# Kernel optimization log

Measured on AMD Instinct MI355X. Metric: run time of the kernel, lower is better.

## Reference

```python
import jax, jax.numpy as jnp
import numpy as np
from jax import lax

MAX_NUM_LEVELS = 3.5
MIN_LEVEL = 0.0
# torch computes num_levels = ceil(levels.max())+1 (data-dependent); since levels are
# clamped to max_num_levels-1 = 2.5, the static upper bound is ceil(2.5)+1 = 4.
# Building the full stack is mathematically identical (gather selects the same levels).
NUM_LEVELS = int(np.ceil(MAX_NUM_LEVELS - 1.0)) + 1  # = 4


def _blur_filter():
    f = np.array([1.0, 3.0, 3.0, 1.0])
    k = f[:, None] * f[None, :]
    k = k / k.sum()
    return jnp.asarray(k, jnp.float32)  # [4,4]


def _downsample_2x(x):
    # reflect-pad 1, depthwise 4x4 Gaussian conv, stride 2  -> [N,C,H/2,W/2]
    N, C, H, W = x.shape
    k = jnp.tile(_blur_filter()[None, None], (C, 1, 1, 1))  # [C,1,4,4]
    xp = jnp.pad(x, ((0, 0), (0, 0), (1, 1), (1, 1)), mode='reflect')
    return lax.conv_general_dilated(xp, k.astype(x.dtype), (2, 2), 'VALID',
                                    feature_group_count=C)


def _upsample(x, scale):
    # bilinear, align_corners=False (half-pixel centers) == jax.image.resize 'bilinear'
    N, C, H, W = x.shape
    return jax.image.resize(x, (N, C, int(H * scale), int(W * scale)), method='bilinear')


def _max_coord_distance(coords):
    # coords [N,H,W,2] -> max neighbor distance [N,H,W] (replication-padded neighbors)
    cp = jnp.pad(coords, ((0, 0), (1, 1), (1, 1), (0, 0)), mode='edge')
    cl = cp[:, 1:-1, :-2]
    cr = cp[:, 1:-1, 2:]
    cu = cp[:, :-2, 1:-1]
    cd = cp[:, 2:, 1:-1]

    def _dist(o):
        sq = jnp.sum((o - coords) ** 2, axis=-1)
        return jnp.sqrt(jnp.clip(sq, 1.0, None))

    return jnp.maximum(jnp.maximum(_dist(cl), _dist(cr)),
                       jnp.maximum(_dist(cu), _dist(cd)))


def _grid_sample_border(img, grid):
    # img [N,K,H,W], grid [N,Ho,Wo,2] in [-1,1]; bilinear, align_corners=False,
    # padding_mode='border' (coords clamped to valid range before interpolation)
    N, K, H, W = img.shape
    ix = jnp.clip(((grid[..., 0] + 1.0) * W - 1.0) / 2.0, 0.0, W - 1.0)
    iy = jnp.clip(((grid[..., 1] + 1.0) * H - 1.0) / 2.0, 0.0, H - 1.0)
    x0f, y0f = jnp.floor(ix), jnp.floor(iy)
    wx = (ix - x0f)[:, None]  # [N,1,Ho,Wo]
    wy = (iy - y0f)[:, None]
    x0 = x0f.astype(jnp.int32)
    y0 = y0f.astype(jnp.int32)
    x1 = jnp.clip(x0 + 1, 0, W - 1)
    y1 = jnp.clip(y0 + 1, 0, H - 1)

    def _gather(im, yi, xi):  # im [K,H,W] -> [K,Ho,Wo]
        return im[:, yi, xi]

    g = jax.vmap(_gather)
    v00 = g(img, y0, x0)
    v01 = g(img, y0, x1)
    v10 = g(img, y1, x0)
    v11 = g(img, y1, x1)
    return (v00 * (1 - wx) + v01 * wx) * (1 - wy) + (v10 * (1 - wx) + v11 * wx) * wy


def setup_inputs() -> dict:
    key = jax.random.key(0)
    k1, k2 = jax.random.split(key)
    N, C, H, W = 4, 96, 256, 256
    inputs = jax.random.normal(k1, (N, C, H, W), dtype=jnp.float32)
    # identity grid + mild random warp -> realistic spread of LOD levels
    ys = (jnp.arange(H, dtype=jnp.float32) + 0.5) / H * 2.0 - 1.0
    xs = (jnp.arange(W, dtype=jnp.float32) + 0.5) / W * 2.0 - 1.0
    gy, gx = jnp.meshgrid(ys, xs, indexing='ij')
    ident = jnp.stack([gx, gy], axis=-1)[None]  # [1,H,W,2]
    noise = (jax.random.uniform(k2, (N, H, W, 2), dtype=jnp.float32) * 2.0 - 1.0) * 0.05
    grid = jnp.clip(ident + noise, -1.0, 1.0)
    return {"inputs": inputs, "grid": grid}


def reference(inputs, grid):
    N, C, H, W = inputs.shape
    Ho, Wo = grid.shape[1], grid.shape[2]
    # absolute-pixel coords of the sampling grid
    xc = (W - 1.0) * (grid[..., 0] + 1.0) / 2.0
    yc = (H - 1.0) * (grid[..., 1] + 1.0) / 2.0
    coords = jnp.stack([xc, yc], axis=-1)  # [N,Ho,Wo,2]
    levels = jnp.clip(jnp.log2(_max_coord_distance(coords)), 0.0, MAX_NUM_LEVELS - 1.0)
    levels = jnp.clip(levels, MIN_LEVEL, None)  # [N,Ho,Wo]

    # Gaussian stack: blur+downsample, then bilinear-upsample back to full res
    lvl_imgs = [inputs]
    cur = inputs
    for i in range(1, NUM_LEVELS):
        cur = _downsample_2x(cur)
        lvl_imgs.append(_upsample(cur, 2.0 ** i))
    stack = jnp.stack(lvl_imgs, axis=2)  # [N,C,D,H,W]
    D = stack.shape[2]

    # warp all levels at once
    warped = _grid_sample_border(stack.reshape(N, C * D, H, W), grid)
    warped = warped.reshape(N, C, D, Ho, Wo)

    # per-pixel trilinear LOD blend
    l0 = jnp.floor(levels).astype(jnp.int32)
    l1 = jnp.ceil(levels).astype(jnp.int32)
    idx0 = jnp.broadcast_to(l0[:, None, None], (N, C, 1, Ho, Wo))
    idx1 = jnp.broadcast_to(l1[:, None, None], (N, C, 1, Ho, Wo))
    o0 = jnp.take_along_axis(warped, idx0, axis=2)[:, :, 0]
    o1 = jnp.take_along_axis(warped, idx1, axis=2)[:, :, 0]
    w = (levels - jnp.floor(levels))[:, None]  # [N,1,Ho,Wo], == levels % 1.0
    return o0 + w * (o1 - o0)
```

## Files before the change

kernel.cpp:

```cpp
#include <hip/hip_runtime.h>
#include <math.h>

namespace {

constexpr int N = 4, C = 96, H = 256, W = 256;
constexpr int HW = H * W;
constexpr float LMAX = 2.5f;

typedef float v4 __attribute__((ext_vector_type(4)));
struct __attribute__((packed, aligned(4))) V4U { v4 v; };
__device__ inline v4 load4u(const float* p) {
  return reinterpret_cast<const V4U*>(p)->v;
}

__global__ __launch_bounds__(256) void levels_kernel(
    const float* __restrict__ grid, float* __restrict__ levels) {
  int idx = blockIdx.x * 256 + threadIdx.x;
  int x = idx & (W - 1);
  int y = (idx >> 8) & (H - 1);
  int n = idx >> 16;
  const float2* gb = reinterpret_cast<const float2*>(grid) + (size_t)n * HW;

  auto cget = [&](int yy, int xx, float& cx, float& cy) {
    yy = min(max(yy, 0), H - 1);
    xx = min(max(xx, 0), W - 1);
    float2 g = gb[yy * W + xx];
    cx = (float)(W - 1) * (g.x + 1.0f) * 0.5f;
    cy = (float)(H - 1) * (g.y + 1.0f) * 0.5f;
  };

  float cx, cy;
  cget(y, x, cx, cy);
  float m = 1.0f;
  const int dxs[4] = {-1, 1, 0, 0};
  const int dys[4] = {0, 0, -1, 1};
#pragma unroll
  for (int i = 0; i < 4; i++) {
    float ox, oy;
    cget(y + dys[i], x + dxs[i], ox, oy);
    float dx = ox - cx, dy = oy - cy;
    m = fmaxf(m, dx * dx + dy * dy);
  }
  float lv = 0.5f * __log2f(m);
  lv = fminf(fmaxf(lv, 0.0f), LMAX);
  levels[idx] = lv;
}

__global__ __launch_bounds__(256) void downsample_tiled(
    const float* __restrict__ in, float* __restrict__ out, int Wi, int T) {
  __shared__ float s[68 * 68];
  int Wo = Wi >> 1;
  int tile = blockIdx.x;
  int nc = blockIdx.y;
  int tx0 = (tile % T) * 32, ty0 = (tile / T) * 32;
  int ix0 = 2 * tx0 - 2, iy0 = 2 * ty0 - 2;
  const float* p = in + (size_t)nc * Wi * Wi;
  int tid = threadIdx.x;

  for (int k = 0; k < 19; k++) {
    int e = tid + 256 * k;
    if (e < 68 * 68) {
      int yy = e / 68, xx = e - 68 * yy;
      int gy = iy0 + yy; gy = gy < 0 ? -gy : (gy >= Wi ? 2 * Wi - 2 - gy : gy);
      int gx = ix0 + xx; gx = gx < 0 ? -gx : (gx >= Wi ? 2 * Wi - 2 - gx : gx);
      s[e] = p[(size_t)gy * Wi + gx];
    }
  }
  __syncthreads();

  const float fw[4] = {0.125f, 0.375f, 0.375f, 0.125f};
  int dx = tid & 31, dy0 = tid >> 5;
  float* po = out + (size_t)nc * Wo * Wo;
#pragma unroll
  for (int r = 0; r < 4; r++) {
    int dy = dy0 + 8 * r;
    float acc = 0.0f;
#pragma unroll
    for (int a = 0; a < 4; a++) {
      const float* row = s + (2 * dy + 1 + a) * 68 + 2 * dx + 1;
      float rsum = fmaf(fw[0], row[0],
                   fmaf(fw[1], row[1],
                   fmaf(fw[2], row[2], fw[3] * row[3])));
      acc = fmaf(fw[a], rsum, acc);
    }
    po[(size_t)(ty0 + dy) * Wo + tx0 + dx] = acc;
  }
}

__device__ inline void axis3(int q0, int q1, float wq, int l, int S,
                             int* ii, float* ww) {
  float inv = 1.0f / (float)(1 << l);
  float pos0 = ((float)q0 + 0.5f) * inv - 0.5f;
  float pos1 = ((float)q1 + 0.5f) * inv - 0.5f;
  int p0 = (int)floorf(pos0), p1 = (int)floorf(pos1);
  float f0 = pos0 - (float)p0, f1 = pos1 - (float)p1;
  int a0 = min(max(p0, 0), S - 1), a1 = min(max(p0 + 1, 0), S - 1);
  int b0 = min(max(p1, 0), S - 1), b1 = min(max(p1 + 1, 0), S - 1);
  int base = min(a0, b0);
  float w0 = 0.f, w1 = 0.f, w2 = 0.f;
  float v; int s;
  v = (1.0f - wq) * (1.0f - f0); s = a0 - base;
  w0 += (s == 0) ? v : 0.f; w1 += (s == 1) ? v : 0.f; w2 += (s == 2) ? v : 0.f;
  v = (1.0f - wq) * f0;          s = a1 - base;
  w0 += (s == 0) ? v : 0.f; w1 += (s == 1) ? v : 0.f; w2 += (s == 2) ? v : 0.f;
  v = wq * (1.0f - f1);          s = b0 - base;
  w0 += (s == 0) ? v : 0.f; w1 += (s == 1) ? v : 0.f; w2 += (s == 2) ? v : 0.f;
  v = wq * f1;                   s = b1 - base;
  w0 += (s == 0) ? v : 0.f; w1 += (s == 1) ? v : 0.f; w2 += (s == 2) ? v : 0.f;
  ii[0] = base;
  ii[1] = min(base + 1, S - 1);
  ii[2] = min(base + 2, S - 1);
  ww[0] = w0; ww[1] = w1; ww[2] = w2;
}

constexpr int L2OFF = 8192, L3OFF = 11392, LDSTOT = 12544;

__global__ __launch_bounds__(256, 3) void gather_tiled(
    const float* __restrict__ inputs, const float* __restrict__ grid,
    const float* __restrict__ levels, const float* __restrict__ pyr1,
    const float* __restrict__ pyr2, const float* __restrict__ pyr3,
    float* __restrict__ out) {
  __shared__ __align__(16) float lds[LDSTOT];
  int tile = blockIdx.x, g = blockIdx.y, n = blockIdx.z;
  int tx0 = (tile & 15) << 4, ty0 = (tile >> 4) << 4;
  int gb = g * 32;
  int tid = threadIdx.x;

  int px = tid & 15, py = tid >> 4;
  int x = tx0 + px, y = ty0 + py;
  int pidx = n * HW + y * W + x;
  float2 gxy = reinterpret_cast<const float2*>(grid)[pidx];
  float lv = levels[pidx];

  int rsx1 = min(max((tx0 >> 1) - 4, 0), 128 - 16);
  int rsy1 = min(max((ty0 >> 1) - 4, 0), 128 - 16);
  int rsx2 = min(max((tx0 >> 2) - 3, 0), 64 - 10);
  int rsy2 = min(max((ty0 >> 2) - 3, 0), 64 - 10);
  int rsx3 = min(max((tx0 >> 3) - 2, 0), 32 - 6);
  int rsy3 = min(max((ty0 >> 3) - 2, 0), 32 - 6);

  {
    const float* base = pyr1 + ((size_t)(n * C + gb)) * (128 * 128);
#pragma unroll
    for (int k = 0; k < 32; k++) {
      int e = tid + 256 * k;
      int c = e >> 8, tf = e & 255;
      int yy = tf >> 4, xx = tf & 15;
      float t = base[(size_t)c * (128 * 128) + (rsy1 + yy) * 128 + rsx1 + xx];
      lds[(c >> 2) * 1024 + tf * 4 + (c & 3)] = t;
    }
  }
  {
    const float* base = pyr2 + ((size_t)(n * C + gb)) * (64 * 64);
    for (int k = 0; k < 13; k++) {
      int e = tid + 256 * k;
      if (e < 3200) {
        int c = e / 100, tf = e - 100 * c;
        int yy = tf / 10, xx = tf - 10 * yy;
        float t = base[(size_t)c * (64 * 64) + (rsy2 + yy) * 64 + rsx2 + xx];
        lds[L2OFF + (c >> 2) * 400 + tf * 4 + (c & 3)] = t;
      }
    }
  }
  {
    const float* base = pyr3 + ((size_t)(n * C + gb)) * (32 * 32);
    for (int k = 0; k < 5; k++) {
      int e = tid + 256 * k;
      if (e < 1152) {
        int c = e / 36, tf = e - 36 * c;
        int yy = tf / 6, xx = tf - 6 * yy;
        float t = base[(size_t)c * (32 * 32) + (rsy3 + yy) * 32 + rsx3 + xx];
        lds[L3OFF + (c >> 2) * 144 + tf * 4 + (c & 3)] = t;
      }
    }
  }
  __syncthreads();

  float ix = fminf(fmaxf(fmaf(gxy.x + 1.0f, 128.0f, -0.5f), 0.0f), 255.0f);
  float iy = fminf(fmaxf(fmaf(gxy.y + 1.0f, 128.0f, -0.5f), 0.0f), 255.0f);
  int x0 = (int)floorf(ix); float wx = ix - (float)x0; int x1 = min(x0 + 1, 255);
  int y0 = (int)floorf(iy); float wy = iy - (float)y0; int y1 = min(y0 + 1, 255);

  float lf = floorf(lv);
  int l0 = (int)lf;
  float wl = lv - lf;
  int lB = l0 + 1;

  auto meta = [&](int l, int& off, int& sz, int& rw, int& rx, int& ry, int& S) {
    if (l == 1)      { off = 0;     sz = 256; rw = 16; rx = rsx1; ry = rsy1; S = 128; }
    else if (l == 2) { off = L2OFF; sz = 100; rw = 10; rx = rsx2; ry = rsy2; S = 64; }
    else             { off = L3OFF; sz = 36;  rw = 6;  rx = rsx3; ry = rsy3; S = 32; }
  };

  int offB, szB, rwB, rxB, ryB, SB;
  meta(lB, offB, szB, rwB, rxB, ryB, SB);
  int tfB[9]; float wB[9];
  {
    int xi[3]; float xw[3]; axis3(x0, x1, wx, lB, SB, xi, xw);
    int yi[3]; float yw[3]; axis3(y0, y1, wy, lB, SB, yi, yw);
#pragma unroll
    for (int r = 0; r < 3; r++)
#pragma unroll
      for (int cc = 0; cc < 3; cc++) {
        int ry_ = min(max(yi[r] - ryB, 0), rwB - 1);
        int rx_ = min(max(xi[cc] - rxB, 0), rwB - 1);
        tfB[r * 3 + cc] = ry_ * rwB + rx_;
        wB[r * 3 + cc] = yw[r] * xw[cc];
      }
  }

  float* po = out + ((size_t)(n * C + gb)) * HW + (size_t)y * W + x;

  if (l0 >= 1) {
    int offA, szA, rwA, rxA, ryA, SA;
    meta(l0, offA, szA, rwA, rxA, ryA, SA);
    int tfA[9]; float wA[9];
    {
      int xi[3]; float xw[3]; axis3(x0, x1, wx, l0, SA, xi, xw);
      int yi[3]; float yw[3]; axis3(y0, y1, wy, l0, SA, yi, yw);
#pragma unroll
      for (int r = 0; r < 3; r++)
#pragma unroll
        for (int cc = 0; cc < 3; cc++) {
          int ry_ = min(max(yi[r] - ryA, 0), rwA - 1);
          int rx_ = min(max(xi[cc] - rxA, 0), rwA - 1);
          tfA[r * 3 + cc] = ry_ * rwA + rx_;
          wA[r * 3 + cc] = yw[r] * xw[cc];
        }
    }
#pragma unroll
    for (int q = 0; q < 8; q++) {
      const float* pA = lds + offA + q * szA * 4;
      const float* pB = lds + offB + q * szB * 4;
      v4 accA = {0.f, 0.f, 0.f, 0.f};
      v4 accB = {0.f, 0.f, 0.f, 0.f};
#pragma unroll
      for (int t = 0; t < 9; t++)
        accA += *reinterpret_cast<const v4*>(pA + tfA[t] * 4) * wA[t];
#pragma unroll
      for (int t = 0; t < 9; t++)
        accB += *reinterpret_cast<const v4*>(pB + tfB[t] * 4) * wB[t];
      v4 o = accA + (accB - accA) * wl;
      float* pq = po + (size_t)(4 * q) * HW;
      pq[0] = o.x; pq[HW] = o.y; pq[2 * (size_t)HW] = o.z; pq[3 * (size_t)HW] = o.w;
    }
  } else {
    const float* inA = inputs + ((size_t)(n * C + gb)) * HW;
#pragma unroll 1
    for (int q = 0; q < 8; q++) {
      const float* pB = lds + offB + q * szB * 4;
      v4 accB = {0.f, 0.f, 0.f, 0.f};
#pragma unroll
      for (int t = 0; t < 9; t++)
        accB += *reinterpret_cast<const v4*>(pB + tfB[t] * 4) * wB[t];
      float av[4];
#pragma unroll
      for (int j = 0; j < 4; j++) {
        const float* ip = inA + (size_t)(4 * q + j) * HW;
        float v00 = ip[y0 * W + x0], v01 = ip[y0 * W + x1];
        float v10 = ip[y1 * W + x0], v11 = ip[y1 * W + x1];
        av[j] = (v00 * (1.f - wx) + v01 * wx) * (1.f - wy) +
                (v10 * (1.f - wx) + v11 * wx) * wy;
      }
      v4 accA = {av[0], av[1], av[2], av[3]};
      v4 o = accA + (accB - accA) * wl;
      float* pq = po + (size_t)(4 * q) * HW;
      pq[0] = o.x; pq[HW] = o.y; pq[2 * (size_t)HW] = o.z; pq[3 * (size_t)HW] = o.w;
    }
  }
}

}

extern "C" void kernel_launch(void* const* d_in, const int* in_sizes, int n_in,
                              void* d_out, int out_size, void* d_ws, size_t ws_size,
                              hipStream_t stream) {
  const float* inputs = (const float*)d_in[0];
  const float* grid = (const float*)d_in[1];
  float* out = (float*)d_out;
  float* ws = (float*)d_ws;

  float* levels = ws;
  float* pyr1 = levels + (size_t)N * HW;
  float* pyr2 = pyr1 + (size_t)N * C * 128 * 128;
  float* pyr3 = pyr2 + (size_t)N * C * 64 * 64;

  int tpix = N * HW;
  levels_kernel<<<tpix / 256, 256, 0, stream>>>(grid, levels);

  int NC = N * C;
  downsample_tiled<<<dim3(16, NC), 256, 0, stream>>>(inputs, pyr1, 256, 4);
  downsample_tiled<<<dim3(4, NC), 256, 0, stream>>>(pyr1, pyr2, 128, 2);
  downsample_tiled<<<dim3(1, NC), 256, 0, stream>>>(pyr2, pyr3, 64, 1);

  gather_tiled<<<dim3(256, 3, N), 256, 0, stream>>>(inputs, grid, levels,
                                                    pyr1, pyr2, pyr3, out);
}
```

Before: 259.7 us.

## Fuse levels into gather, merge pyramid levels 2-3, vectorize level-1 loads

```diff
diff --git a/kernel.cpp b/kernel.cpp
--- a/kernel.cpp
+++ b/kernel.cpp
@@ -12,58 +12,36 @@
 __device__ inline v4 load4u(const float* p) {
   return reinterpret_cast<const V4U*>(p)->v;
 }
-
-__global__ __launch_bounds__(256) void levels_kernel(
-    const float* __restrict__ grid, float* __restrict__ levels) {
-  int idx = blockIdx.x * 256 + threadIdx.x;
-  int x = idx & (W - 1);
-  int y = (idx >> 8) & (H - 1);
-  int n = idx >> 16;
-  const float2* gb = reinterpret_cast<const float2*>(grid) + (size_t)n * HW;
-
-  auto cget = [&](int yy, int xx, float& cx, float& cy) {
-    yy = min(max(yy, 0), H - 1);
-    xx = min(max(xx, 0), W - 1);
-    float2 g = gb[yy * W + xx];
-    cx = (float)(W - 1) * (g.x + 1.0f) * 0.5f;
-    cy = (float)(H - 1) * (g.y + 1.0f) * 0.5f;
-  };
-
-  float cx, cy;
-  cget(y, x, cx, cy);
-  float m = 1.0f;
-  const int dxs[4] = {-1, 1, 0, 0};
-  const int dys[4] = {0, 0, -1, 1};
-#pragma unroll
-  for (int i = 0; i < 4; i++) {
-    float ox, oy;
-    cget(y + dys[i], x + dxs[i], ox, oy);
-    float dx = ox - cx, dy = oy - cy;
-    m = fmaxf(m, dx * dx + dy * dy);
-  }
-  float lv = 0.5f * __log2f(m);
-  lv = fminf(fmaxf(lv, 0.0f), LMAX);
-  levels[idx] = lv;
-}
-
-__global__ __launch_bounds__(256) void downsample_tiled(
-    const float* __restrict__ in, float* __restrict__ out, int Wi, int T) {
+__device__ inline int refl(int i, int S) {
+  i = i < 0 ? -i : i;
+  return i >= S ? 2 * S - 2 - i : i;
+}
+
+__global__ __launch_bounds__(256) void downsample1(
+    const float* __restrict__ in, float* __restrict__ out) {
   __shared__ float s[68 * 68];
-  int Wo = Wi >> 1;
-  int tile = blockIdx.x;
-  int nc = blockIdx.y;
+  const int Wi = 256, Wo = 128, T = 4;
+  int tile = blockIdx.x, nc = blockIdx.y;
   int tx0 = (tile % T) * 32, ty0 = (tile / T) * 32;
   int ix0 = 2 * tx0 - 2, iy0 = 2 * ty0 - 2;
   const float* p = in + (size_t)nc * Wi * Wi;
   int tid = threadIdx.x;
 
-  for (int k = 0; k < 19; k++) {
-    int e = tid + 256 * k;
-    if (e < 68 * 68) {
-      int yy = e / 68, xx = e - 68 * yy;
-      int gy = iy0 + yy; gy = gy < 0 ? -gy : (gy >= Wi ? 2 * Wi - 2 - gy : gy);
-      int gx = ix0 + xx; gx = gx < 0 ? -gx : (gx >= Wi ? 2 * Wi - 2 - gx : gx);
-      s[e] = p[(size_t)gy * Wi + gx];
+  for (int k = 0; k < 5; k++) {
+    int ch = tid + 256 * k;
+    if (ch < 68 * 17) {
+      int yy = ch / 17, cx = (ch - 17 * yy) * 4;
+      int gy = refl(iy0 + yy, Wi);
+      int gx = ix0 + cx;
+      const float* rowp = p + (size_t)gy * Wi;
+      float* sp = s + yy * 68 + cx;
+      if (gx >= 0 && gx + 3 < Wi) {
+        v4 t = load4u(rowp + gx);
+        sp[0] = t.x; sp[1] = t.y; sp[2] = t.z; sp[3] = t.w;
+      } else {
+#pragma unroll
+        for (int j = 0; j < 4; j++) sp[j] = rowp[refl(gx + j, Wi)];
+      }
     }
   }
   __syncthreads();
@@ -78,12 +56,96 @@
 #pragma unroll
     for (int a = 0; a < 4; a++) {
       const float* row = s + (2 * dy + 1 + a) * 68 + 2 * dx + 1;
-      float rsum = fmaf(fw[0], row[0],
-                   fmaf(fw[1], row[1],
-                   fmaf(fw[2], row[2], fw[3] * row[3])));
-      acc = fmaf(fw[a], rsum, acc);
+      acc = fmaf(fw[a],
+                 fmaf(fw[0], row[0],
+                 fmaf(fw[1], row[1],
+                 fmaf(fw[2], row[2], fw[3] * row[3]))), acc);
     }
     po[(size_t)(ty0 + dy) * Wo + tx0 + dx] = acc;
+  }
+}
+
+__global__ __launch_bounds__(256) void downsample23(
+    const float* __restrict__ pyr1, float* __restrict__ pyr2,
+    float* __restrict__ pyr3) {
+  __shared__ float s1[70 * 72];
+  __shared__ float h2[70 * 36];
+  __shared__ float p2[34 * 36];
+  __shared__ float h3[34 * 16];
+  int t = blockIdx.x, nc = blockIdx.y;
+  int t3x = (t & 1) * 16, t3y = (t >> 1) * 16;
+  int u0x = 2 * t3x - 1, u0y = 2 * t3y - 1;
+  int v0x = 2 * u0x - 1, v0y = 2 * u0y - 1;
+  const float* p1 = pyr1 + (size_t)nc * 128 * 128;
+  int tid = threadIdx.x;
+  const float fw[4] = {0.125f, 0.375f, 0.375f, 0.125f};
+
+  for (int k = 0; k < 20; k++) {
+    int e = tid + 256 * k;
+    if (e < 4900) {
+      int yy = e / 70, xx = e - 70 * yy;
+      s1[yy * 72 + xx] =
+          p1[(size_t)refl(v0y + yy, 128) * 128 + refl(v0x + xx, 128)];
+    }
+  }
+  __syncthreads();
+
+  for (int k = 0; k < 10; k++) {
+    int e = tid + 256 * k;
+    if (e < 70 * 34) {
+      int r = e / 34, c = e - 34 * r;
+      const float* sp = s1 + r * 72 + 2 * c;
+      h2[r * 36 + c] = fmaf(fw[0], sp[0],
+                       fmaf(fw[1], sp[1],
+                       fmaf(fw[2], sp[2], fw[3] * sp[3])));
+    }
+  }
+  __syncthreads();
+
+  for (int k = 0; k < 5; k++) {
+    int e = tid + 256 * k;
+    if (e < 34 * 34) {
+      int r = e / 34, c = e - 34 * r;
+      const float* hp = h2 + (2 * r) * 36 + c;
+      p2[r * 36 + c] = fmaf(fw[0], hp[0],
+                       fmaf(fw[1], hp[36],
+                       fmaf(fw[2], hp[72], fw[3] * hp[108])));
+    }
+  }
+  __syncthreads();
+
+  float* o2 = pyr2 + (size_t)nc * 64 * 64;
+#pragma unroll
+  for (int k = 0; k < 4; k++) {
+    int e = tid + 256 * k;
+    int yy = e >> 5, xx = e & 31;
+    o2[(size_t)(2 * t3y + yy) * 64 + 2 * t3x + xx] = p2[(yy + 1) * 36 + xx + 1];
+  }
+
+  for (int k = 0; k < 3; k++) {
+    int e = tid + 256 * k;
+    if (e < 34 * 16) {
+      int r = e >> 4, c = e & 15;
+      float acc = 0.f;
+#pragma unroll
+      for (int kk = 0; kk < 4; kk++) {
+        int j = refl(2 * (t3x + c) - 1 + kk, 64) - u0x;
+        acc = fmaf(fw[kk], p2[r * 36 + j], acc);
+      }
+      h3[r * 16 + c] = acc;
+    }
+  }
+  __syncthreads();
+
+  {
+    int yy = tid >> 4, xx = tid & 15;
+    float acc = 0.f;
+#pragma unroll
+    for (int kk = 0; kk < 4; kk++) {
+      int j = refl(2 * (t3y + yy) - 1 + kk, 64) - u0y;
+      acc = fmaf(fw[kk], h3[j * 16 + xx], acc);
+    }
+    pyr3[(size_t)nc * 32 * 32 + (t3y + yy) * 32 + t3x + xx] = acc;
   }
 }
 
@@ -117,9 +179,8 @@
 
 __global__ __launch_bounds__(256, 3) void gather_tiled(
     const float* __restrict__ inputs, const float* __restrict__ grid,
-    const float* __restrict__ levels, const float* __restrict__ pyr1,
-    const float* __restrict__ pyr2, const float* __restrict__ pyr3,
-    float* __restrict__ out) {
+    const float* __restrict__ pyr1, const float* __restrict__ pyr2,
+    const float* __restrict__ pyr3, float* __restrict__ out) {
   __shared__ __align__(16) float lds[LDSTOT];
   int tile = blockIdx.x, g = blockIdx.y, n = blockIdx.z;
   int tx0 = (tile & 15) << 4, ty0 = (tile >> 4) << 4;
@@ -128,9 +189,13 @@
 
   int px = tid & 15, py = tid >> 4;
   int x = tx0 + px, y = ty0 + py;
-  int pidx = n * HW + y * W + x;
-  float2 gxy = reinterpret_cast<const float2*>(grid)[pidx];
-  float lv = levels[pidx];
+
+  const float2* gp = reinterpret_cast<const float2*>(grid) + (size_t)n * HW;
+  float2 gc = gp[y * W + x];
+  float2 gl = gp[y * W + max(x - 1, 0)];
+  float2 gr = gp[y * W + min(x + 1, W - 1)];
+  float2 gu = gp[max(y - 1, 0) * W + x];
+  float2 gd = gp[min(y + 1, H - 1) * W + x];
 
   int rsx1 = min(max((tx0 >> 1) - 4, 0), 128 - 16);
   int rsy1 = min(max((ty0 >> 1) - 4, 0), 128 - 16);
@@ -176,14 +241,30 @@
   }
   __syncthreads();
 
-  float ix = fminf(fmaxf(fmaf(gxy.x + 1.0f, 128.0f, -0.5f), 0.0f), 255.0f);
-  float iy = fminf(fmaxf(fmaf(gxy.y + 1.0f, 128.0f, -0.5f), 0.0f), 255.0f);
+  float lv;
+  {
+    float cx = 255.0f * (gc.x + 1.0f) * 0.5f;
+    float cy = 255.0f * (gc.y + 1.0f) * 0.5f;
+    float m = 1.0f;
+    float2 nb[4] = {gl, gr, gu, gd};
+#pragma unroll
+    for (int i = 0; i < 4; i++) {
+      float ox = 255.0f * (nb[i].x + 1.0f) * 0.5f - cx;
+      float oy = 255.0f * (nb[i].y + 1.0f) * 0.5f - cy;
+      m = fmaxf(m, ox * ox + oy * oy);
+    }
+    lv = fminf(fmaxf(0.5f * __log2f(m), 0.0f), LMAX);
+  }
+
+  float ix = fminf(fmaxf(fmaf(gc.x + 1.0f, 128.0f, -0.5f), 0.0f), 255.0f);
+  float iy = fminf(fmaxf(fmaf(gc.y + 1.0f, 128.0f, -0.5f), 0.0f), 255.0f);
   int x0 = (int)floorf(ix); float wx = ix - (float)x0; int x1 = min(x0 + 1, 255);
   int y0 = (int)floorf(iy); float wy = iy - (float)y0; int y1 = min(y0 + 1, 255);
 
   float lf = floorf(lv);
   int l0 = (int)lf;
   float wl = lv - lf;
+  float wlA = 1.0f - wl;
   int lB = l0 + 1;
 
   auto meta = [&](int l, int& off, int& sz, int& rw, int& rx, int& ry, int& S) {
@@ -205,7 +286,7 @@
         int ry_ = min(max(yi[r] - ryB, 0), rwB - 1);
         int rx_ = min(max(xi[cc] - rxB, 0), rwB - 1);
         tfB[r * 3 + cc] = ry_ * rwB + rx_;
-        wB[r * 3 + cc] = yw[r] * xw[cc];
+        wB[r * 3 + cc] = yw[r] * xw[cc] * wl;
       }
   }
 
@@ -225,24 +306,23 @@
           int ry_ = min(max(yi[r] - ryA, 0), rwA - 1);
           int rx_ = min(max(xi[cc] - rxA, 0), rwA - 1);
           tfA[r * 3 + cc] = ry_ * rwA + rx_;
-          wA[r * 3 + cc] = yw[r] * xw[cc];
+          wA[r * 3 + cc] = yw[r] * xw[cc] * wlA;
         }
     }
 #pragma unroll
     for (int q = 0; q < 8; q++) {
       const float* pA = lds + offA + q * szA * 4;
       const float* pB = lds + offB + q * szB * 4;
-      v4 accA = {0.f, 0.f, 0.f, 0.f};
-      v4 accB = {0.f, 0.f, 0.f, 0.f};
+      v4 acc = {0.f, 0.f, 0.f, 0.f};
 #pragma unroll
       for (int t = 0; t < 9; t++)
-        accA += *reinterpret_cast<const v4*>(pA + tfA[t] * 4) * wA[t];
+        acc += *reinterpret_cast<const v4*>(pA + tfA[t] * 4) * wA[t];
 #pragma unroll
       for (int t = 0; t < 9; t++)
-        accB += *reinterpret_cast<const v4*>(pB + tfB[t] * 4) * wB[t];
-      v4 o = accA + (accB - accA) * wl;
+        acc += *reinterpret_cast<const v4*>(pB + tfB[t] * 4) * wB[t];
       float* pq = po + (size_t)(4 * q) * HW;
-      pq[0] = o.x; pq[HW] = o.y; pq[2 * (size_t)HW] = o.z; pq[3 * (size_t)HW] = o.w;
+      pq[0] = acc.x; pq[HW] = acc.y;
+      pq[2 * (size_t)HW] = acc.z; pq[3 * (size_t)HW] = acc.w;
     }
   } else {
     const float* inA = inputs + ((size_t)(n * C + gb)) * HW;
@@ -262,10 +342,11 @@
         av[j] = (v00 * (1.f - wx) + v01 * wx) * (1.f - wy) +
                 (v10 * (1.f - wx) + v11 * wx) * wy;
       }
-      v4 accA = {av[0], av[1], av[2], av[3]};
-      v4 o = accA + (accB - accA) * wl;
+      v4 o = {fmaf(av[0], wlA, accB.x), fmaf(av[1], wlA, accB.y),
+              fmaf(av[2], wlA, accB.z), fmaf(av[3], wlA, accB.w)};
       float* pq = po + (size_t)(4 * q) * HW;
-      pq[0] = o.x; pq[HW] = o.y; pq[2 * (size_t)HW] = o.z; pq[3 * (size_t)HW] = o.w;
+      pq[0] = o.x; pq[HW] = o.y;
+      pq[2 * (size_t)HW] = o.z; pq[3 * (size_t)HW] = o.w;
     }
   }
 }
@@ -280,19 +361,13 @@
   float* out = (float*)d_out;
   float* ws = (float*)d_ws;
 
-  float* levels = ws;
-  float* pyr1 = levels + (size_t)N * HW;
+  float* pyr1 = ws;
   float* pyr2 = pyr1 + (size_t)N * C * 128 * 128;
   float* pyr3 = pyr2 + (size_t)N * C * 64 * 64;
 
-  int tpix = N * HW;
-  levels_kernel<<<tpix / 256, 256, 0, stream>>>(grid, levels);
-
   int NC = N * C;
-  downsample_tiled<<<dim3(16, NC), 256, 0, stream>>>(inputs, pyr1, 256, 4);
-  downsample_tiled<<<dim3(4, NC), 256, 0, stream>>>(pyr1, pyr2, 128, 2);
-  downsample_tiled<<<dim3(1, NC), 256, 0, stream>>>(pyr2, pyr3, 64, 1);
-
-  gather_tiled<<<dim3(256, 3, N), 256, 0, stream>>>(inputs, grid, levels,
+  downsample1<<<dim3(16, NC), 256, 0, stream>>>(inputs, pyr1);
+  downsample23<<<dim3(4, NC), 256, 0, stream>>>(pyr1, pyr2, pyr3);
+  gather_tiled<<<dim3(256, 3, N), 256, 0, stream>>>(inputs, grid,
                                                     pyr1, pyr2, pyr3, out);
 }
```

After: 256.2 us. About the same (-1.4%).
